# Kernel tuning notes

Hardware: AMD Instinct MI355X
Metric: run time of the kernel (lower is better)

## Reference

```python
import jax, jax.numpy as jnp
import numpy as np

U, I, E, T = 60000, 30000, 64, 2000
N = U + I
ADJ_NNZ = 1_600_000
UI_NNZ = 800_000
TAGS_PER_ITEM = 4


def setup_inputs() -> dict:
    key = jax.random.key(0)
    ks = jax.random.split(key, 8)
    # LightGCN normalized adjacency in COO form (values already normalized offline)
    adj_rows = jax.random.randint(ks[0], (ADJ_NNZ,), 0, N, dtype=jnp.int32)
    adj_cols = jax.random.randint(ks[1], (ADJ_NNZ,), 0, N, dtype=jnp.int32)
    adj_vals = jax.random.uniform(ks[2], (ADJ_NNZ,), dtype=jnp.float32) * 0.01
    # Item-tag incidence H: 4 distinct tags per item (binary incidence, no duplicates)
    items_np = np.repeat(np.arange(I, dtype=np.int32), TAGS_PER_ITEM)
    tags_np = ((np.arange(I, dtype=np.int64)[:, None] * 7919 + np.arange(TAGS_PER_ITEM)[None, :] * 131) % T).astype(np.int32).reshape(-1)
    h_items = jnp.asarray(items_np)
    h_tags = jnp.asarray(tags_np)
    # Row-normalized user-item interaction matrix (D_u^-1 @ trn_mat) in COO form
    ui_rows = jax.random.randint(ks[3], (UI_NNZ,), 0, U, dtype=jnp.int32)
    ui_cols = jax.random.randint(ks[4], (UI_NNZ,), 0, I, dtype=jnp.int32)
    ui_vals = jax.random.uniform(ks[5], (UI_NNZ,), dtype=jnp.float32) * 0.01
    return {
        'user_embeds': jax.random.normal(ks[6], (U, E), dtype=jnp.float32) * 0.1,
        'item_embeds': jax.random.normal(jax.random.fold_in(ks[6], 1), (I, E), dtype=jnp.float32) * 0.1,
        'hypergraph_user_embeds': jax.random.normal(ks[7], (U, E), dtype=jnp.float32) * 0.1,
        'hypergraph_item_embeds': jax.random.normal(jax.random.fold_in(ks[7], 1), (I, E), dtype=jnp.float32) * 0.1,
        'adj_rows': adj_rows, 'adj_cols': adj_cols, 'adj_vals': adj_vals,
        'h_items': h_items, 'h_tags': h_tags,
        'ui_rows': ui_rows, 'ui_cols': ui_cols, 'ui_vals': ui_vals,
        'layer_num': 3,
    }


def _spmm(rows, cols, vals, x, n):
    # y[r] += vals[e] * x[cols[e]] for each edge e with rows[e]==r  (t.spmm)
    return jax.ops.segment_sum(vals[:, None] * x[cols], rows, num_segments=n)


def reference(user_embeds, item_embeds, hypergraph_user_embeds, hypergraph_item_embeds,
              adj_rows, adj_cols, adj_vals, h_items, h_tags, ui_rows, ui_cols, ui_vals,
              layer_num):
    ones = jnp.ones(h_items.shape[0], dtype=user_embeds.dtype)
    # B: hyperedge (tag) degree; D: item degree; zero degrees clamped to 1
    B = jax.ops.segment_sum(ones, h_tags, num_segments=T)
    D = jax.ops.segment_sum(ones, h_items, num_segments=I)
    B_inv = 1.0 / jnp.where(B == 0, 1.0, B)
    D_inv = 1.0 / jnp.where(D == 0, 1.0, D)

    def hconv(x):  # D^-1 H B^-1 H^T x, never materializing the item x item adjacency
        y = jax.ops.segment_sum(x[h_items], h_tags, num_segments=T) * B_inv[:, None]
        z = jax.ops.segment_sum(y[h_tags], h_items, num_segments=I)
        return z * D_inv[:, None]

    # LightGCN propagation: sum of all layer embeddings (layer 0 included)
    cur = jnp.concatenate([user_embeds, item_embeds], axis=0)  # [N, E]
    acc = cur
    for _ in range(layer_num):
        cur = _spmm(adj_rows, adj_cols, adj_vals, cur, N)
        acc = acc + cur

    # Hypergraph propagation on items
    hcur = hypergraph_item_embeds
    hacc = hcur
    for _ in range(layer_num):
        hcur = hconv(hcur)
        hacc = hacc + hcur

    # Hypergraph user embeds: own params + degree-normalized sum of interacted items
    hg_user = hypergraph_user_embeds + _spmm(ui_rows, ui_cols, ui_vals, hacc, U)

    return acc[:U], acc[U:], hg_user, hacc
```

## Files before the change

### kernel.cpp

```cpp
#include <hip/hip_runtime.h>

#define E 64
#define TQ 16
#define RPB 256
#define RPB_SHIFT 8
#define NBMAX 1024
#define CHUNK_C 4096
#define CHUNK_P 4096
#define FP8_SCALE 512.0f
#define FP8_INV   (1.0f / 512.0f)

static inline int nblk(long n, int bs) { return (int)((n + bs - 1) / bs); }


__device__ __forceinline__ unsigned short f2bf(float f) {
    unsigned u = __float_as_uint(f);
    u += 0x7FFF + ((u >> 16) & 1);
    return (unsigned short)(u >> 16);
}
__device__ __forceinline__ float bf2f(unsigned short h) {
    return __uint_as_float((unsigned)h << 16);
}
__device__ __forceinline__ int f2v15(float f) {
    unsigned u = __float_as_uint(f);
    u += 0x7FFF + ((u >> 16) & 1);
    return (int)((u >> 16) & 0x7FFF);
}
__device__ __forceinline__ float v15f(int p) {
    return __uint_as_float(((unsigned)p >> 17) << 16);
}
__device__ __forceinline__ int pack_fp8x4(float4 v) {
    int w = __builtin_amdgcn_cvt_pk_fp8_f32(v.x, v.y, 0, false);
    w = __builtin_amdgcn_cvt_pk_fp8_f32(v.z, v.w, w, true);
    return w;
}


__global__ void __launch_bounds__(512)
k_count_cvt(const int* __restrict__ adj_rows, int nadj,
            const int* __restrict__ ui_rows, int nui,
            const int* __restrict__ h_tags,
            int* __restrict__ bucket_cnt, int OFF_UI, int OFF_TAG, int NB, int ET,
            const float4* __restrict__ ua, const float4* __restrict__ ub,
            int splitv4, int* __restrict__ xf8, int ncvt, int CB) {
    __shared__ int h4[4][NBMAX];
    if ((int)blockIdx.x < CB) {
        for (int b = threadIdx.x; b < 4 * NBMAX; b += 512) ((int*)h4)[b] = 0;
        __syncthreads();
        int c = (threadIdx.x >> 4) & 3;
        int start = blockIdx.x * CHUNK_C;
        int end = start + CHUNK_C; if (end > ET) end = ET;
        for (int i = start + (int)threadIdx.x; i < end; i += 512) {
            int row;
            if (i < nadj) row = adj_rows[i];
            else if (i < nadj + nui) row = OFF_UI + ui_rows[i - nadj];
            else row = OFF_TAG + h_tags[i - nadj - nui];
            atomicAdd(&h4[c][row >> RPB_SHIFT], 1);
        }
        __syncthreads();
        for (int b = threadIdx.x; b < NB; b += 512) {
            int tot = h4[0][b] + h4[1][b] + h4[2][b] + h4[3][b];
            if (tot) atomicAdd(&bucket_cnt[b], tot);
        }
    } else {
        int i = ((int)blockIdx.x - CB) * 512 + threadIdx.x;
        if (i < ncvt) {
            float4 v = (i < splitv4) ? ua[i] : ub[i - splitv4];
            v.x *= FP8_SCALE; v.y *= FP8_SCALE; v.z *= FP8_SCALE; v.w *= FP8_SCALE;
            xf8[i] = pack_fp8x4(v);
        }
    }
}


__global__ void __launch_bounds__(1024)
k_scan_nb(const int* __restrict__ cnt, int* __restrict__ base, int* __restrict__ bcur,
          int* __restrict__ rp, int M, int NB, int ET) {
    __shared__ int sh[1024];
    int tid = threadIdx.x;
    int v = (tid < NB) ? cnt[tid] : 0;
    sh[tid] = v;
    __syncthreads();
    for (int off = 1; off < 1024; off <<= 1) {
        int t = (tid >= off) ? sh[tid - off] : 0;
        __syncthreads();
        sh[tid] += t;
        __syncthreads();
    }
    if (tid < NB) {
        int excl = sh[tid] - v;
        base[tid] = excl;
        bcur[tid] = excl;
        if (tid == NB - 1) base[NB] = sh[tid];
    }
    if (tid == 0) rp[M] = ET;
}


__global__ void __launch_bounds__(512)
k_partition(const int* __restrict__ adj_rows, const int* __restrict__ adj_cols,
            const float* __restrict__ adj_vals, int nadj,
            const int* __restrict__ ui_rows, const int* __restrict__ ui_cols,
            const float* __restrict__ ui_vals, int nui,
            const int* __restrict__ h_tags, const int* __restrict__ h_items,
            int* __restrict__ bcur, int2* __restrict__ staged,
            int OFF_UI, int OFF_TAG, int NB, int ET) {
    __shared__ int h4[4][NBMAX];
    for (int b = threadIdx.x; b < 4 * NBMAX; b += 512) ((int*)h4)[b] = 0;
    __syncthreads();

    int c = (threadIdx.x >> 4) & 3;
    int start = blockIdx.x * CHUNK_P;

    int rowA[8], colA[8], vbA[8];
    #pragma unroll
    for (int k = 0; k < 8; ++k) {
        int i = start + k * 512 + (int)threadIdx.x;
        int row = -1, col = 0, vb = 0;
        if (i < ET) {
            if (i < nadj) {
                row = adj_rows[i]; col = adj_cols[i]; vb = f2v15(adj_vals[i]);
            } else if (i < nadj + nui) {
                int j = i - nadj;
                row = OFF_UI + ui_rows[j]; col = ui_cols[j]; vb = f2v15(ui_vals[j]);
            } else {
                int j = i - nadj - nui;
                row = OFF_TAG + h_tags[j]; col = h_items[j]; vb = 0;
            }
            atomicAdd(&h4[c][row >> RPB_SHIFT], 1);
        }
        rowA[k] = row; colA[k] = col; vbA[k] = vb;
    }
    __syncthreads();

    for (int b = threadIdx.x; b < NB; b += 512) {
        int c0 = h4[0][b], c1 = h4[1][b], c2 = h4[2][b], c3 = h4[3][b];
        int tot = c0 + c1 + c2 + c3;
        if (tot) {
            int g = atomicAdd(&bcur[b], tot);
            h4[0][b] = g;
            h4[1][b] = g + c0;
            h4[2][b] = g + c0 + c1;
            h4[3][b] = g + c0 + c1 + c2;
        }
    }
    __syncthreads();

    #pragma unroll
    for (int k = 0; k < 8; ++k) {
        if (rowA[k] >= 0) {
            int b = rowA[k] >> RPB_SHIFT;
            int pos = atomicAdd(&h4[c][b], 1);
            staged[pos] = make_int2(((rowA[k] & (RPB - 1)) << 17) | colA[k], vbA[k]);
        }
    }
}


__global__ void __launch_bounds__(512)
k_bucket_csr(const int2* __restrict__ staged, const int* __restrict__ bbase,
             int* __restrict__ rp, int* __restrict__ pool, int M) {
    __shared__ int h4[4][RPB];
    __shared__ int scn[RPB];
    int b = blockIdx.x;
    int s0 = bbase[b], s1 = bbase[b + 1];
    for (int i = threadIdx.x; i < 4 * RPB; i += 512) ((int*)h4)[i] = 0;
    __syncthreads();
    int c = (threadIdx.x >> 4) & 3;
    for (int e = s0 + (int)threadIdx.x; e < s1; e += 512) {
        int lrow = ((unsigned)staged[e].x) >> 17;
        atomicAdd(&h4[c][lrow], 1);
    }
    __syncthreads();
    int tot = (threadIdx.x < RPB)
        ? h4[0][threadIdx.x] + h4[1][threadIdx.x] + h4[2][threadIdx.x] + h4[3][threadIdx.x] : 0;
    if (threadIdx.x < RPB) scn[threadIdx.x] = tot;
    __syncthreads();
    for (int off = 1; off < RPB; off <<= 1) {
        int t = 0;
        if (threadIdx.x < RPB && (int)threadIdx.x >= off) t = scn[threadIdx.x - off];
        __syncthreads();
        if (threadIdx.x < RPB) scn[threadIdx.x] += t;
        __syncthreads();
    }
    int row0 = b << RPB_SHIFT;
    if (threadIdx.x < RPB) {
        int excl = s0 + scn[threadIdx.x] - tot;
        if (row0 + (int)threadIdx.x < M) rp[row0 + threadIdx.x] = excl;
        int c0 = h4[0][threadIdx.x], c1 = h4[1][threadIdx.x], c2 = h4[2][threadIdx.x];
        h4[0][threadIdx.x] = excl;
        h4[1][threadIdx.x] = excl + c0;
        h4[2][threadIdx.x] = excl + c0 + c1;
        h4[3][threadIdx.x] = excl + c0 + c1 + c2;
    }
    __syncthreads();
    for (int e = s0 + (int)threadIdx.x; e < s1; e += 512) {
        int2 ed = staged[e];
        int lrow = ((unsigned)ed.x) >> 17;
        int pos = atomicAdd(&h4[c][lrow], 1);
        pool[pos] = (ed.y << 17) | (ed.x & 0x1FFFF);
    }
}


__global__ void k_spmm_fp8(const int* __restrict__ rp, const int* __restrict__ pool,
                           const int* __restrict__ xf8, int* __restrict__ yf8, int n) {
    int gid = blockIdx.x * blockDim.x + threadIdx.x;
    int row = gid >> 4;
    if (row >= n) return;
    int q = gid & 15;
    int s0 = rp[row], s1 = rp[row + 1];
    float4 s = make_float4(0.f, 0.f, 0.f, 0.f);
    int e = s0;
    for (; e + 4 <= s1; e += 4) {
        int p0 = pool[e], p1 = pool[e + 1], p2 = pool[e + 2], p3 = pool[e + 3];
        int w0 = xf8[(long)(p0 & 0x1FFFF) * TQ + q];
        int w1 = xf8[(long)(p1 & 0x1FFFF) * TQ + q];
        int w2 = xf8[(long)(p2 & 0x1FFFF) * TQ + q];
        int w3 = xf8[(long)(p3 & 0x1FFFF) * TQ + q];
        float v0 = v15f(p0), v1 = v15f(p1), v2 = v15f(p2), v3 = v15f(p3);
        s.x += v0 * __builtin_amdgcn_cvt_f32_fp8(w0, 0);
        s.y += v0 * __builtin_amdgcn_cvt_f32_fp8(w0, 1);
        s.z += v0 * __builtin_amdgcn_cvt_f32_fp8(w0, 2);
        s.w += v0 * __builtin_amdgcn_cvt_f32_fp8(w0, 3);
        s.x += v1 * __builtin_amdgcn_cvt_f32_fp8(w1, 0);
        s.y += v1 * __builtin_amdgcn_cvt_f32_fp8(w1, 1);
        s.z += v1 * __builtin_amdgcn_cvt_f32_fp8(w1, 2);
        s.w += v1 * __builtin_amdgcn_cvt_f32_fp8(w1, 3);
        s.x += v2 * __builtin_amdgcn_cvt_f32_fp8(w2, 0);
        s.y += v2 * __builtin_amdgcn_cvt_f32_fp8(w2, 1);
        s.z += v2 * __builtin_amdgcn_cvt_f32_fp8(w2, 2);
        s.w += v2 * __builtin_amdgcn_cvt_f32_fp8(w2, 3);
        s.x += v3 * __builtin_amdgcn_cvt_f32_fp8(w3, 0);
        s.y += v3 * __builtin_amdgcn_cvt_f32_fp8(w3, 1);
        s.z += v3 * __builtin_amdgcn_cvt_f32_fp8(w3, 2);
        s.w += v3 * __builtin_amdgcn_cvt_f32_fp8(w3, 3);
    }
    for (; e < s1; ++e) {
        int p0 = pool[e];
        int w0 = xf8[(long)(p0 & 0x1FFFF) * TQ + q];
        float v0 = v15f(p0);
        s.x += v0 * __builtin_amdgcn_cvt_f32_fp8(w0, 0);
        s.y += v0 * __builtin_amdgcn_cvt_f32_fp8(w0, 1);
        s.z += v0 * __builtin_amdgcn_cvt_f32_fp8(w0, 2);
        s.w += v0 * __builtin_amdgcn_cvt_f32_fp8(w0, 3);
    }
    yf8[(long)row * TQ + q] = pack_fp8x4(s);
}


__global__ void __launch_bounds__(256)
k_tag_final(const int* __restrict__ rp, int rp_off, const int* __restrict__ pool,
            const float* __restrict__ x, float* __restrict__ y, int ntags, int TB,
            const float4* __restrict__ ua, const float4* __restrict__ ub, int splitv4,
            const int* __restrict__ l1, const int* __restrict__ l2,
            const int* __restrict__ l3, float4* __restrict__ acc, int n4) {
    if ((int)blockIdx.x < TB) {
        int t = (blockIdx.x * 256 + threadIdx.x) >> 6;
        if (t >= ntags) return;
        int lane = threadIdx.x & 63;
        int q = lane & 15;
        int g = lane >> 4;
        int s0 = rp[rp_off + t], s1 = rp[rp_off + t + 1];
        float4 s = make_float4(0.f, 0.f, 0.f, 0.f);
        for (int e = s0 + g; e < s1; e += 4) {
            int it = pool[e] & 0x1FFFF;
            float4 xv = ((const float4*)x)[(long)it * TQ + q];
            s.x += xv.x; s.y += xv.y; s.z += xv.z; s.w += xv.w;
        }
        s.x += __shfl_xor(s.x, 16, 64); s.y += __shfl_xor(s.y, 16, 64);
        s.z += __shfl_xor(s.z, 16, 64); s.w += __shfl_xor(s.w, 16, 64);
        s.x += __shfl_xor(s.x, 32, 64); s.y += __shfl_xor(s.y, 32, 64);
        s.z += __shfl_xor(s.z, 32, 64); s.w += __shfl_xor(s.w, 32, 64);
        if (g == 0) {
            int b = s1 - s0;
            float binv = (b > 0) ? (1.f / (float)b) : 1.f;
            s.x *= binv; s.y *= binv; s.z *= binv; s.w *= binv;
            ((float4*)y)[(long)t * TQ + q] = s;
        }
    } else {
        int i = ((int)blockIdx.x - TB) * 256 + threadIdx.x;
        if (i >= n4) return;
        float4 a = (i < splitv4) ? ua[i] : ub[i - splitv4];
        int w1 = l1[i], w2 = l2[i], w3 = l3[i];
        a.x += (__builtin_amdgcn_cvt_f32_fp8(w1, 0) + __builtin_amdgcn_cvt_f32_fp8(w2, 0)
                + __builtin_amdgcn_cvt_f32_fp8(w3, 0)) * FP8_INV;
        a.y += (__builtin_amdgcn_cvt_f32_fp8(w1, 1) + __builtin_amdgcn_cvt_f32_fp8(w2, 1)
                + __builtin_amdgcn_cvt_f32_fp8(w3, 1)) * FP8_INV;
        a.z += (__builtin_amdgcn_cvt_f32_fp8(w1, 2) + __builtin_amdgcn_cvt_f32_fp8(w2, 2)
                + __builtin_amdgcn_cvt_f32_fp8(w3, 2)) * FP8_INV;
        a.w += (__builtin_amdgcn_cvt_f32_fp8(w1, 3) + __builtin_amdgcn_cvt_f32_fp8(w2, 3)
                + __builtin_amdgcn_cvt_f32_fp8(w3, 3)) * FP8_INV;
        acc[i] = a;
    }
}


__global__ void __launch_bounds__(256)
k_tag_gather(const int* __restrict__ rp, int rp_off,
             const int* __restrict__ pool, const float* __restrict__ x,
             float* __restrict__ y, int ntags) {
    int t = (blockIdx.x * 256 + threadIdx.x) >> 6;
    if (t >= ntags) return;
    int lane = threadIdx.x & 63;
    int q = lane & 15;
    int g = lane >> 4;
    int s0 = rp[rp_off + t], s1 = rp[rp_off + t + 1];
    float4 s = make_float4(0.f, 0.f, 0.f, 0.f);
    for (int e = s0 + g; e < s1; e += 4) {
        int it = pool[e] & 0x1FFFF;
        float4 xv = ((const float4*)x)[(long)it * TQ + q];
        s.x += xv.x; s.y += xv.y; s.z += xv.z; s.w += xv.w;
    }
    s.x += __shfl_xor(s.x, 16, 64); s.y += __shfl_xor(s.y, 16, 64);
    s.z += __shfl_xor(s.z, 16, 64); s.w += __shfl_xor(s.w, 16, 64);
    s.x += __shfl_xor(s.x, 32, 64); s.y += __shfl_xor(s.y, 32, 64);
    s.z += __shfl_xor(s.z, 32, 64); s.w += __shfl_xor(s.w, 32, 64);
    if (g == 0) {
        int b = s1 - s0;
        float binv = (b > 0) ? (1.f / (float)b) : 1.f;
        s.x *= binv; s.y *= binv; s.z *= binv; s.w *= binv;
        ((float4*)y)[(long)t * TQ + q] = s;
    }
}

__global__ void k_gather_items(const int* __restrict__ h_tags, const float* __restrict__ y,
                               const float* __restrict__ init, float* __restrict__ hcur,
                               float* __restrict__ hacc, ushort4* __restrict__ hacc_bf,
                               int nitems, int K, int mode, int wn) {
    int gid = blockIdx.x * blockDim.x + threadIdx.x;
    int i = gid >> 4;
    if (i >= nitems) return;
    int q = gid & 15;
    float4 s = make_float4(0.f, 0.f, 0.f, 0.f);
    if (K == 4) {
        int4 t4 = ((const int4*)h_tags)[i];
        float4 y0 = ((const float4*)y)[(long)t4.x * TQ + q];
        float4 y1 = ((const float4*)y)[(long)t4.y * TQ + q];
        float4 y2 = ((const float4*)y)[(long)t4.z * TQ + q];
        float4 y3 = ((const float4*)y)[(long)t4.w * TQ + q];
        s.x = (y0.x + y1.x) + (y2.x + y3.x);
        s.y = (y0.y + y1.y) + (y2.y + y3.y);
        s.z = (y0.z + y1.z) + (y2.z + y3.z);
        s.w = (y0.w + y1.w) + (y2.w + y3.w);
    } else {
        for (int k = 0; k < K; ++k) {
            int t = h_tags[(long)i * K + k];
            float4 yv = ((const float4*)y)[(long)t * TQ + q];
            s.x += yv.x; s.y += yv.y; s.z += yv.z; s.w += yv.w;
        }
    }
    float dinv = 1.f / (float)K;
    s.x *= dinv; s.y *= dinv; s.z *= dinv; s.w *= dinv;
    long o = (long)i * TQ + q;
    if (wn) ((float4*)hcur)[o] = s;
    float4 a;
    if (mode == 0) a = ((const float4*)init)[o];
    else           a = ((const float4*)hacc)[o];
    a.x += s.x; a.y += s.y; a.z += s.z; a.w += s.w;
    ((float4*)hacc)[o] = a;
    if (hacc_bf) {
        ushort4 hb;
        hb.x = f2bf(a.x); hb.y = f2bf(a.y); hb.z = f2bf(a.z); hb.w = f2bf(a.w);
        hacc_bf[o] = hb;
    }
}


__global__ void k_csr_spmm_base_bf(const int* __restrict__ rp, int rp_off,
                                   const int* __restrict__ pool,
                                   const ushort4* __restrict__ xbf,
                                   const float* __restrict__ base,
                                   float* __restrict__ out, int n) {
    int gid = blockIdx.x * blockDim.x + threadIdx.x;
    int row = gid >> 4;
    if (row >= n) return;
    int q = gid & 15;
    int s0 = rp[rp_off + row], s1 = rp[rp_off + row + 1];
    float4 s = make_float4(0.f, 0.f, 0.f, 0.f);
    int e = s0;
    for (; e + 4 <= s1; e += 4) {
        int p0 = pool[e], p1 = pool[e + 1], p2 = pool[e + 2], p3 = pool[e + 3];
        ushort4 h0 = xbf[(long)(p0 & 0x1FFFF) * TQ + q];
        ushort4 h1 = xbf[(long)(p1 & 0x1FFFF) * TQ + q];
        ushort4 h2 = xbf[(long)(p2 & 0x1FFFF) * TQ + q];
        ushort4 h3 = xbf[(long)(p3 & 0x1FFFF) * TQ + q];
        float v0 = v15f(p0), v1 = v15f(p1), v2 = v15f(p2), v3 = v15f(p3);
        s.x += v0 * bf2f(h0.x); s.y += v0 * bf2f(h0.y);
        s.z += v0 * bf2f(h0.z); s.w += v0 * bf2f(h0.w);
        s.x += v1 * bf2f(h1.x); s.y += v1 * bf2f(h1.y);
        s.z += v1 * bf2f(h1.z); s.w += v1 * bf2f(h1.w);
        s.x += v2 * bf2f(h2.x); s.y += v2 * bf2f(h2.y);
        s.z += v2 * bf2f(h2.z); s.w += v2 * bf2f(h2.w);
        s.x += v3 * bf2f(h3.x); s.y += v3 * bf2f(h3.y);
        s.z += v3 * bf2f(h3.z); s.w += v3 * bf2f(h3.w);
    }
    for (; e < s1; ++e) {
        int p0 = pool[e];
        ushort4 h0 = xbf[(long)(p0 & 0x1FFFF) * TQ + q];
        float v0 = v15f(p0);
        s.x += v0 * bf2f(h0.x); s.y += v0 * bf2f(h0.y);
        s.z += v0 * bf2f(h0.z); s.w += v0 * bf2f(h0.w);
    }
    long o = (long)row * TQ + q;
    float4 bv = ((const float4*)base)[o];
    bv.x += s.x; bv.y += s.y; bv.z += s.z; bv.w += s.w;
    ((float4*)out)[o] = bv;
}


extern "C" void kernel_launch(void* const* d_in, const int* in_sizes, int n_in,
                              void* d_out, int out_size, void* d_ws, size_t ws_size,
                              hipStream_t stream) {
    const float* user_embeds = (const float*)d_in[0];
    const float* item_embeds = (const float*)d_in[1];
    const float* hyper_user  = (const float*)d_in[2];
    const float* hyper_item  = (const float*)d_in[3];
    const int*   adj_rows    = (const int*)d_in[4];
    const int*   adj_cols    = (const int*)d_in[5];
    const float* adj_vals    = (const float*)d_in[6];
    const int*   h_items     = (const int*)d_in[7];
    const int*   h_tags      = (const int*)d_in[8];
    const int*   ui_rows     = (const int*)d_in[9];
    const int*   ui_cols     = (const int*)d_in[10];
    const float* ui_vals     = (const float*)d_in[11];

    const int U = in_sizes[0] / E;
    const int I = in_sizes[1] / E;
    const int N = U + I;
    const int ADJ = in_sizes[4];
    const int NH  = in_sizes[7];
    const int UI  = in_sizes[9];
    const int K   = NH / I;
    const int T   = 2000;
    const int ET  = ADJ + UI + NH;

    const int OFF_UI  = (N + RPB - 1) & ~(RPB - 1);
    const int OFF_TAG = (OFF_UI + U + RPB - 1) & ~(RPB - 1);
    const int M   = OFF_TAG + T;
    const int NB  = (M + RPB - 1) >> RPB_SHIFT;

    float* out     = (float*)d_out;
    float* acc     = out;
    float* hg_user = out + (size_t)N * E;
    float* hacc    = hg_user + (size_t)U * E;

    char* ws = (char*)d_ws;
    auto alloc = [&](size_t bytes) { char* p = ws; ws += (bytes + 255) & ~(size_t)255; return p; };

    int*  xf0 = (int*)alloc((size_t)N * TQ * sizeof(int));
    int*  xf1 = (int*)alloc((size_t)N * TQ * sizeof(int));
    int*  xf2 = (int*)alloc((size_t)N * TQ * sizeof(int));
    int*  xf3 = (int*)alloc((size_t)N * TQ * sizeof(int));
    int2* staged = (int2*)alloc((size_t)ET * sizeof(int2));
    float* hcur    = (float*)alloc((size_t)I * E * sizeof(float));
    float* y       = (float*)alloc((size_t)T * E * sizeof(float));
    unsigned short* hacc_bf = (unsigned short*)alloc((size_t)I * E * sizeof(unsigned short));
    int*   pool    = (int*)alloc((size_t)ET * sizeof(int));
    int*   rp      = (int*)alloc((size_t)(M + 1) * sizeof(int));
    int*   bcnt    = (int*)alloc((size_t)NBMAX * sizeof(int));
    int*   bbase   = (int*)alloc((size_t)(NBMAX + 1) * sizeof(int));
    int*   bcur    = (int*)alloc((size_t)NBMAX * sizeof(int));

    const int BS = 256;
    const int TAG_BLOCKS = nblk((long)T * 64, 256);
    const int CB = nblk(ET, CHUNK_C);
    const int CVB = nblk((long)N * TQ, 512);
    const int FSB = nblk((long)N * TQ, 256);

    hipMemsetAsync(bcnt, 0, (size_t)NB * sizeof(int), stream);
    k_count_cvt<<<CB + CVB, 512, 0, stream>>>(
        adj_rows, ADJ, ui_rows, UI, h_tags, bcnt, OFF_UI, OFF_TAG, NB, ET,
        (const float4*)user_embeds, (const float4*)item_embeds, U * TQ,
        xf0, N * TQ, CB);
    k_scan_nb<<<1, 1024, 0, stream>>>(bcnt, bbase, bcur, rp, M, NB, ET);
    k_partition<<<nblk(ET, CHUNK_P), 512, 0, stream>>>(
        adj_rows, adj_cols, adj_vals, ADJ, ui_rows, ui_cols, ui_vals, UI,
        h_tags, h_items, bcur, staged, OFF_UI, OFF_TAG, NB, ET);
    k_bucket_csr<<<NB, 512, 0, stream>>>(staged, bbase, rp, pool, M);

    k_spmm_fp8<<<nblk((long)N * TQ, BS), BS, 0, stream>>>(rp, pool, xf0, xf1, N);
    k_spmm_fp8<<<nblk((long)N * TQ, BS), BS, 0, stream>>>(rp, pool, xf1, xf2, N);
    k_spmm_fp8<<<nblk((long)N * TQ, BS), BS, 0, stream>>>(rp, pool, xf2, xf3, N);

    k_tag_final<<<TAG_BLOCKS + FSB, 256, 0, stream>>>(
        rp, OFF_TAG, pool, hyper_item, y, T, TAG_BLOCKS,
        (const float4*)user_embeds, (const float4*)item_embeds, U * TQ,
        xf1, xf2, xf3, (float4*)acc, N * TQ);

    k_gather_items<<<nblk((long)I * TQ, BS), BS, 0, stream>>>(
        h_tags, y, hyper_item, hcur, hacc, nullptr, I, K, 0, 1);
    k_tag_gather<<<TAG_BLOCKS, 256, 0, stream>>>(rp, OFF_TAG, pool, hcur, y, T);
    k_gather_items<<<nblk((long)I * TQ, BS), BS, 0, stream>>>(
        h_tags, y, nullptr, hcur, hacc, nullptr, I, K, 1, 1);
    k_tag_gather<<<TAG_BLOCKS, 256, 0, stream>>>(rp, OFF_TAG, pool, hcur, y, T);
    k_gather_items<<<nblk((long)I * TQ, BS), BS, 0, stream>>>(
        h_tags, y, nullptr, hcur, hacc, (ushort4*)hacc_bf, I, K, 1, 0);

    k_csr_spmm_base_bf<<<nblk((long)U * TQ, BS), BS, 0, stream>>>(
        rp, OFF_UI, pool, (const ushort4*)hacc_bf, hyper_user, hg_user, U);
}
```

Measured before the change: 361.5 us.

## Reformulate hypergraph propagation in tag space and overlap it with adjacency SpMM

The hypergraph layers are recomputed in tag space. Each hop gathers tag vectors through the item's tags, and the three tag-level results are summed so items only gather once at the end. The tag hops are launched as extra blocks inside the three LightGCN SpMM launches, and the final item gather is merged with the layer-sum kernel. This removes several dependent small launches and the per-item intermediate buffers, cutting serialized kernel count. In exchange, each tag hop does K-fold gathers per item, and the summation order changes slightly.

```diff
diff --git a/kernel.cpp b/kernel.cpp
--- a/kernel.cpp
+++ b/kernel.cpp
@@ -203,9 +203,11 @@
 }
 
 
-__global__ void k_spmm_fp8(const int* __restrict__ rp, const int* __restrict__ pool,
-                           const int* __restrict__ xf8, int* __restrict__ yf8, int n) {
-    int gid = blockIdx.x * blockDim.x + threadIdx.x;
+__device__ __forceinline__ void spmm_body(const int* __restrict__ rp,
+                                          const int* __restrict__ pool,
+                                          const int* __restrict__ xf8,
+                                          int* __restrict__ yf8, int n, int bid) {
+    int gid = bid * 256 + (int)threadIdx.x;
     int row = gid >> 4;
     if (row >= n) return;
     int q = gid & 15;
@@ -248,38 +250,163 @@
     yf8[(long)row * TQ + q] = pack_fp8x4(s);
 }
 
-
-__global__ void __launch_bounds__(256)
-k_tag_final(const int* __restrict__ rp, int rp_off, const int* __restrict__ pool,
-            const float* __restrict__ x, float* __restrict__ y, int ntags, int TB,
-            const float4* __restrict__ ua, const float4* __restrict__ ub, int splitv4,
-            const int* __restrict__ l1, const int* __restrict__ l2,
-            const int* __restrict__ l3, float4* __restrict__ acc, int n4) {
-    if ((int)blockIdx.x < TB) {
-        int t = (blockIdx.x * 256 + threadIdx.x) >> 6;
-        if (t >= ntags) return;
-        int lane = threadIdx.x & 63;
-        int q = lane & 15;
-        int g = lane >> 4;
-        int s0 = rp[rp_off + t], s1 = rp[rp_off + t + 1];
-        float4 s = make_float4(0.f, 0.f, 0.f, 0.f);
+__device__ __forceinline__ void tag_hop_body(const int* __restrict__ rp, int rp_off,
+                                             const int* __restrict__ pool,
+                                             const float* __restrict__ x,
+                                             float* __restrict__ y, int ntags, int bid) {
+    int t = (bid * 256 + (int)threadIdx.x) >> 6;
+    if (t >= ntags) return;
+    int lane = threadIdx.x & 63;
+    int q = lane & 15;
+    int g = lane >> 4;
+    int s0 = rp[rp_off + t], s1 = rp[rp_off + t + 1];
+    float4 s = make_float4(0.f, 0.f, 0.f, 0.f);
+    for (int e = s0 + g; e < s1; e += 4) {
+        int it = pool[e] & 0x1FFFF;
+        float4 xv = ((const float4*)x)[(long)it * TQ + q];
+        s.x += xv.x; s.y += xv.y; s.z += xv.z; s.w += xv.w;
+    }
+    s.x += __shfl_xor(s.x, 16, 64); s.y += __shfl_xor(s.y, 16, 64);
+    s.z += __shfl_xor(s.z, 16, 64); s.w += __shfl_xor(s.w, 16, 64);
+    s.x += __shfl_xor(s.x, 32, 64); s.y += __shfl_xor(s.y, 32, 64);
+    s.z += __shfl_xor(s.z, 32, 64); s.w += __shfl_xor(s.w, 32, 64);
+    if (g == 0) {
+        int b = s1 - s0;
+        float binv = (b > 0) ? (1.f / (float)b) : 1.f;
+        s.x *= binv; s.y *= binv; s.z *= binv; s.w *= binv;
+        ((float4*)y)[(long)t * TQ + q] = s;
+    }
+}
+
+__device__ __forceinline__ void tag_g_body(const int* __restrict__ rp, int rp_off,
+                                           const int* __restrict__ pool,
+                                           const int* __restrict__ tags, int K,
+                                           const float* __restrict__ yin,
+                                           const float* __restrict__ yprev,
+                                           float* __restrict__ yout, int ntags, int bid) {
+    int t = (bid * 256 + (int)threadIdx.x) >> 6;
+    if (t >= ntags) return;
+    int lane = threadIdx.x & 63;
+    int q = lane & 15;
+    int g = lane >> 4;
+    int s0 = rp[rp_off + t], s1 = rp[rp_off + t + 1];
+    float4 s = make_float4(0.f, 0.f, 0.f, 0.f);
+    if (K == 4) {
         for (int e = s0 + g; e < s1; e += 4) {
             int it = pool[e] & 0x1FFFF;
-            float4 xv = ((const float4*)x)[(long)it * TQ + q];
-            s.x += xv.x; s.y += xv.y; s.z += xv.z; s.w += xv.w;
-        }
-        s.x += __shfl_xor(s.x, 16, 64); s.y += __shfl_xor(s.y, 16, 64);
-        s.z += __shfl_xor(s.z, 16, 64); s.w += __shfl_xor(s.w, 16, 64);
-        s.x += __shfl_xor(s.x, 32, 64); s.y += __shfl_xor(s.y, 32, 64);
-        s.z += __shfl_xor(s.z, 32, 64); s.w += __shfl_xor(s.w, 32, 64);
-        if (g == 0) {
-            int b = s1 - s0;
-            float binv = (b > 0) ? (1.f / (float)b) : 1.f;
-            s.x *= binv; s.y *= binv; s.z *= binv; s.w *= binv;
-            ((float4*)y)[(long)t * TQ + q] = s;
+            int4 t4 = ((const int4*)tags)[it];
+            float4 a0 = ((const float4*)yin)[(long)t4.x * TQ + q];
+            float4 a1 = ((const float4*)yin)[(long)t4.y * TQ + q];
+            float4 a2 = ((const float4*)yin)[(long)t4.z * TQ + q];
+            float4 a3 = ((const float4*)yin)[(long)t4.w * TQ + q];
+            s.x += (a0.x + a1.x) + (a2.x + a3.x);
+            s.y += (a0.y + a1.y) + (a2.y + a3.y);
+            s.z += (a0.z + a1.z) + (a2.z + a3.z);
+            s.w += (a0.w + a1.w) + (a2.w + a3.w);
         }
     } else {
-        int i = ((int)blockIdx.x - TB) * 256 + threadIdx.x;
+        for (int e = s0 + g; e < s1; e += 4) {
+            int it = pool[e] & 0x1FFFF;
+            for (int k = 0; k < K; ++k) {
+                int tt = tags[(long)it * K + k];
+                float4 a = ((const float4*)yin)[(long)tt * TQ + q];
+                s.x += a.x; s.y += a.y; s.z += a.z; s.w += a.w;
+            }
+        }
+    }
+    s.x += __shfl_xor(s.x, 16, 64); s.y += __shfl_xor(s.y, 16, 64);
+    s.z += __shfl_xor(s.z, 16, 64); s.w += __shfl_xor(s.w, 16, 64);
+    s.x += __shfl_xor(s.x, 32, 64); s.y += __shfl_xor(s.y, 32, 64);
+    s.z += __shfl_xor(s.z, 32, 64); s.w += __shfl_xor(s.w, 32, 64);
+    if (g == 0) {
+        int b = s1 - s0;
+        float dinv = 1.f / (float)K;
+        float f = (b > 0) ? (dinv / (float)b) : 0.f;
+        s.x *= f; s.y *= f; s.z *= f; s.w *= f;
+        long o = (long)t * TQ + q;
+        if (yprev) {
+            float4 p1 = ((const float4*)yprev)[o];
+            float4 p2 = ((const float4*)yin)[o];
+            s.x += p1.x + p2.x; s.y += p1.y + p2.y;
+            s.z += p1.z + p2.z; s.w += p1.w + p2.w;
+        }
+        ((float4*)yout)[o] = s;
+    }
+}
+
+__device__ __forceinline__ void items_body(const int* __restrict__ tags, int K,
+                                           const float* __restrict__ ysum,
+                                           const float* __restrict__ init,
+                                           float* __restrict__ hacc,
+                                           ushort4* __restrict__ hacc_bf,
+                                           int nitems, int bid) {
+    int gid = bid * 256 + (int)threadIdx.x;
+    int i = gid >> 4;
+    if (i >= nitems) return;
+    int q = gid & 15;
+    float4 s = make_float4(0.f, 0.f, 0.f, 0.f);
+    if (K == 4) {
+        int4 t4 = ((const int4*)tags)[i];
+        float4 y0 = ((const float4*)ysum)[(long)t4.x * TQ + q];
+        float4 y1 = ((const float4*)ysum)[(long)t4.y * TQ + q];
+        float4 y2 = ((const float4*)ysum)[(long)t4.z * TQ + q];
+        float4 y3 = ((const float4*)ysum)[(long)t4.w * TQ + q];
+        s.x = (y0.x + y1.x) + (y2.x + y3.x);
+        s.y = (y0.y + y1.y) + (y2.y + y3.y);
+        s.z = (y0.z + y1.z) + (y2.z + y3.z);
+        s.w = (y0.w + y1.w) + (y2.w + y3.w);
+    } else {
+        for (int k = 0; k < K; ++k) {
+            int tt = tags[(long)i * K + k];
+            float4 yv = ((const float4*)ysum)[(long)tt * TQ + q];
+            s.x += yv.x; s.y += yv.y; s.z += yv.z; s.w += yv.w;
+        }
+    }
+    float dinv = 1.f / (float)K;
+    s.x *= dinv; s.y *= dinv; s.z *= dinv; s.w *= dinv;
+    long o = (long)i * TQ + q;
+    float4 a = ((const float4*)init)[o];
+    a.x += s.x; a.y += s.y; a.z += s.z; a.w += s.w;
+    ((float4*)hacc)[o] = a;
+    ushort4 hb;
+    hb.x = f2bf(a.x); hb.y = f2bf(a.y); hb.z = f2bf(a.z); hb.w = f2bf(a.w);
+    hacc_bf[o] = hb;
+}
+
+
+__global__ void __launch_bounds__(256)
+k_spmm_tag(const int* __restrict__ rp, const int* __restrict__ pool,
+           const int* __restrict__ xf8, int* __restrict__ yf8, int n, int SB,
+           int rp_off, const float* __restrict__ xtag, float* __restrict__ y1,
+           int ntags) {
+    if ((int)blockIdx.x < SB)
+        spmm_body(rp, pool, xf8, yf8, n, blockIdx.x);
+    else
+        tag_hop_body(rp, rp_off, pool, xtag, y1, ntags, (int)blockIdx.x - SB);
+}
+
+__global__ void __launch_bounds__(256)
+k_spmm_g(const int* __restrict__ rp, const int* __restrict__ pool,
+         const int* __restrict__ xf8, int* __restrict__ yf8, int n, int SB,
+         int rp_off, const int* __restrict__ tags, int K,
+         const float* __restrict__ yin, const float* __restrict__ yprev,
+         float* __restrict__ yout, int ntags) {
+    if ((int)blockIdx.x < SB)
+        spmm_body(rp, pool, xf8, yf8, n, blockIdx.x);
+    else
+        tag_g_body(rp, rp_off, pool, tags, K, yin, yprev, yout, ntags,
+                   (int)blockIdx.x - SB);
+}
+
+__global__ void __launch_bounds__(256)
+k_final_items(const float4* __restrict__ ua, const float4* __restrict__ ub,
+              int splitv4, const int* __restrict__ l1, const int* __restrict__ l2,
+              const int* __restrict__ l3, float4* __restrict__ acc, int n4, int FSB,
+              const int* __restrict__ tags, int K, const float* __restrict__ ysum,
+              const float* __restrict__ hyper_item, float* __restrict__ hacc,
+              ushort4* __restrict__ hacc_bf, int nitems) {
+    if ((int)blockIdx.x < FSB) {
+        int i = (int)blockIdx.x * 256 + threadIdx.x;
         if (i >= n4) return;
         float4 a = (i < splitv4) ? ua[i] : ub[i - splitv4];
         int w1 = l1[i], w2 = l2[i], w3 = l3[i];
@@ -292,77 +419,9 @@
         a.w += (__builtin_amdgcn_cvt_f32_fp8(w1, 3) + __builtin_amdgcn_cvt_f32_fp8(w2, 3)
                 + __builtin_amdgcn_cvt_f32_fp8(w3, 3)) * FP8_INV;
         acc[i] = a;
-    }
-}
-
-
-__global__ void __launch_bounds__(256)
-k_tag_gather(const int* __restrict__ rp, int rp_off,
-             const int* __restrict__ pool, const float* __restrict__ x,
-             float* __restrict__ y, int ntags) {
-    int t = (blockIdx.x * 256 + threadIdx.x) >> 6;
-    if (t >= ntags) return;
-    int lane = threadIdx.x & 63;
-    int q = lane & 15;
-    int g = lane >> 4;
-    int s0 = rp[rp_off + t], s1 = rp[rp_off + t + 1];
-    float4 s = make_float4(0.f, 0.f, 0.f, 0.f);
-    for (int e = s0 + g; e < s1; e += 4) {
-        int it = pool[e] & 0x1FFFF;
-        float4 xv = ((const float4*)x)[(long)it * TQ + q];
-        s.x += xv.x; s.y += xv.y; s.z += xv.z; s.w += xv.w;
-    }
-    s.x += __shfl_xor(s.x, 16, 64); s.y += __shfl_xor(s.y, 16, 64);
-    s.z += __shfl_xor(s.z, 16, 64); s.w += __shfl_xor(s.w, 16, 64);
-    s.x += __shfl_xor(s.x, 32, 64); s.y += __shfl_xor(s.y, 32, 64);
-    s.z += __shfl_xor(s.z, 32, 64); s.w += __shfl_xor(s.w, 32, 64);
-    if (g == 0) {
-        int b = s1 - s0;
-        float binv = (b > 0) ? (1.f / (float)b) : 1.f;
-        s.x *= binv; s.y *= binv; s.z *= binv; s.w *= binv;
-        ((float4*)y)[(long)t * TQ + q] = s;
-    }
-}
-
-__global__ void k_gather_items(const int* __restrict__ h_tags, const float* __restrict__ y,
-                               const float* __restrict__ init, float* __restrict__ hcur,
-                               float* __restrict__ hacc, ushort4* __restrict__ hacc_bf,
-                               int nitems, int K, int mode, int wn) {
-    int gid = blockIdx.x * blockDim.x + threadIdx.x;
-    int i = gid >> 4;
-    if (i >= nitems) return;
-    int q = gid & 15;
-    float4 s = make_float4(0.f, 0.f, 0.f, 0.f);
-    if (K == 4) {
-        int4 t4 = ((const int4*)h_tags)[i];
-        float4 y0 = ((const float4*)y)[(long)t4.x * TQ + q];
-        float4 y1 = ((const float4*)y)[(long)t4.y * TQ + q];
-        float4 y2 = ((const float4*)y)[(long)t4.z * TQ + q];
-        float4 y3 = ((const float4*)y)[(long)t4.w * TQ + q];
-        s.x = (y0.x + y1.x) + (y2.x + y3.x);
-        s.y = (y0.y + y1.y) + (y2.y + y3.y);
-        s.z = (y0.z + y1.z) + (y2.z + y3.z);
-        s.w = (y0.w + y1.w) + (y2.w + y3.w);
     } else {
-        for (int k = 0; k < K; ++k) {
-            int t = h_tags[(long)i * K + k];
-            float4 yv = ((const float4*)y)[(long)t * TQ + q];
-            s.x += yv.x; s.y += yv.y; s.z += yv.z; s.w += yv.w;
-        }
-    }
-    float dinv = 1.f / (float)K;
-    s.x *= dinv; s.y *= dinv; s.z *= dinv; s.w *= dinv;
-    long o = (long)i * TQ + q;
-    if (wn) ((float4*)hcur)[o] = s;
-    float4 a;
-    if (mode == 0) a = ((const float4*)init)[o];
-    else           a = ((const float4*)hacc)[o];
-    a.x += s.x; a.y += s.y; a.z += s.z; a.w += s.w;
-    ((float4*)hacc)[o] = a;
-    if (hacc_bf) {
-        ushort4 hb;
-        hb.x = f2bf(a.x); hb.y = f2bf(a.y); hb.z = f2bf(a.z); hb.w = f2bf(a.w);
-        hacc_bf[o] = hb;
+        items_body(tags, K, ysum, hyper_item, hacc, hacc_bf, nitems,
+                   (int)blockIdx.x - FSB);
     }
 }
 
@@ -453,8 +512,9 @@
     int*  xf2 = (int*)alloc((size_t)N * TQ * sizeof(int));
     int*  xf3 = (int*)alloc((size_t)N * TQ * sizeof(int));
     int2* staged = (int2*)alloc((size_t)ET * sizeof(int2));
-    float* hcur    = (float*)alloc((size_t)I * E * sizeof(float));
-    float* y       = (float*)alloc((size_t)T * E * sizeof(float));
+    float* y1      = (float*)alloc((size_t)T * E * sizeof(float));
+    float* y2      = (float*)alloc((size_t)T * E * sizeof(float));
+    float* ys      = (float*)alloc((size_t)T * E * sizeof(float));
     unsigned short* hacc_bf = (unsigned short*)alloc((size_t)I * E * sizeof(unsigned short));
     int*   pool    = (int*)alloc((size_t)ET * sizeof(int));
     int*   rp      = (int*)alloc((size_t)(M + 1) * sizeof(int));
@@ -464,9 +524,11 @@
 
     const int BS = 256;
     const int TAG_BLOCKS = nblk((long)T * 64, 256);
-    const int CB = nblk(ET, CHUNK_C);
+    const int CB  = nblk(ET, CHUNK_C);
     const int CVB = nblk((long)N * TQ, 512);
-    const int FSB = nblk((long)N * TQ, 256);
+    const int SB  = nblk((long)N * TQ, BS);
+    const int FSB = nblk((long)N * TQ, BS);
+    const int IB  = nblk((long)I * TQ, BS);
 
     hipMemsetAsync(bcnt, 0, (size_t)NB * sizeof(int), stream);
     k_count_cvt<<<CB + CVB, 512, 0, stream>>>(
@@ -479,23 +541,17 @@
         h_tags, h_items, bcur, staged, OFF_UI, OFF_TAG, NB, ET);
     k_bucket_csr<<<NB, 512, 0, stream>>>(staged, bbase, rp, pool, M);
 
-    k_spmm_fp8<<<nblk((long)N * TQ, BS), BS, 0, stream>>>(rp, pool, xf0, xf1, N);
-    k_spmm_fp8<<<nblk((long)N * TQ, BS), BS, 0, stream>>>(rp, pool, xf1, xf2, N);
-    k_spmm_fp8<<<nblk((long)N * TQ, BS), BS, 0, stream>>>(rp, pool, xf2, xf3, N);
-
-    k_tag_final<<<TAG_BLOCKS + FSB, 256, 0, stream>>>(
-        rp, OFF_TAG, pool, hyper_item, y, T, TAG_BLOCKS,
+    k_spmm_tag<<<SB + TAG_BLOCKS, BS, 0, stream>>>(
+        rp, pool, xf0, xf1, N, SB, OFF_TAG, hyper_item, y1, T);
+    k_spmm_g<<<SB + TAG_BLOCKS, BS, 0, stream>>>(
+        rp, pool, xf1, xf2, N, SB, OFF_TAG, h_tags, K, y1, nullptr, y2, T);
+    k_spmm_g<<<SB + TAG_BLOCKS, BS, 0, stream>>>(
+        rp, pool, xf2, xf3, N, SB, OFF_TAG, h_tags, K, y2, y1, ys, T);
+
+    k_final_items<<<FSB + IB, BS, 0, stream>>>(
         (const float4*)user_embeds, (const float4*)item_embeds, U * TQ,
-        xf1, xf2, xf3, (float4*)acc, N * TQ);
-
-    k_gather_items<<<nblk((long)I * TQ, BS), BS, 0, stream>>>(
-        h_tags, y, hyper_item, hcur, hacc, nullptr, I, K, 0, 1);
-    k_tag_gather<<<TAG_BLOCKS, 256, 0, stream>>>(rp, OFF_TAG, pool, hcur, y, T);
-    k_gather_items<<<nblk((long)I * TQ, BS), BS, 0, stream>>>(
-        h_tags, y, nullptr, hcur, hacc, nullptr, I, K, 1, 1);
-    k_tag_gather<<<TAG_BLOCKS, 256, 0, stream>>>(rp, OFF_TAG, pool, hcur, y, T);
-    k_gather_items<<<nblk((long)I * TQ, BS), BS, 0, stream>>>(
-        h_tags, y, nullptr, hcur, hacc, (ushort4*)hacc_bf, I, K, 1, 0);
+        xf1, xf2, xf3, (float4*)acc, N * TQ, FSB,
+        h_tags, K, ys, hyper_item, hacc, (ushort4*)hacc_bf, I);
 
     k_csr_spmm_base_bf<<<nblk((long)U * TQ, BS), BS, 0, stream>>>(
         rp, OFF_UI, pool, (const ushort4*)hacc_bf, hyper_user, hg_user, U);
```

After: 333.8 us. 7.7% less time.
